# Optimization experiments

Hardware: AMD Instinct MI355X
Metric: run time of the kernel (lower is better)

## Reference

```python
import jax, jax.numpy as jnp
import numpy as np

D_MODEL = 256
N_LEVELS = 4
N_HEADS = 8
N_POINTS = 4
D_HEAD = D_MODEL // N_HEADS  # 32
BATCH = 8
SHAPES = np.array([[64, 64], [32, 32], [16, 16], [8, 8]], dtype=np.int32)
LEN_IN = int((SHAPES[:, 0] * SHAPES[:, 1]).sum())  # 5440
LEN_Q = LEN_IN
STARTS = np.concatenate([[0], np.cumsum(SHAPES[:, 0] * SHAPES[:, 1])[:-1]]).astype(np.int32)


def _offset_bias():
    # faithful _reset_parameters grid init for sampling_offsets bias
    thetas = np.arange(N_HEADS, dtype=np.float64) * (2.0 * np.pi / N_HEADS)
    grid = np.stack([np.cos(thetas), np.sin(thetas)], -1)
    grid = grid / np.abs(grid).max(-1, keepdims=True)
    grid = np.tile(grid[:, None, None, :], (1, N_LEVELS, N_POINTS, 1))
    grid = grid * (np.arange(N_POINTS) + 1)[None, None, :, None]
    return jnp.asarray(grid.reshape(-1), dtype=jnp.float32)


def setup_inputs() -> dict:
    key = jax.random.key(0)
    ks = jax.random.split(key, 8)
    s = 1.0 / np.sqrt(D_MODEL)
    return {
        "query": jax.random.normal(ks[0], (BATCH, LEN_Q, D_MODEL), jnp.float32),
        "reference_points": jax.random.uniform(ks[1], (BATCH, LEN_Q, N_LEVELS, 2), jnp.float32),
        "input_flatten": jax.random.normal(ks[2], (BATCH, LEN_IN, D_MODEL), jnp.float32),
        "input_spatial_shapes": jnp.asarray(SHAPES),
        "input_level_start_index": jnp.asarray(STARTS),
        "W_val": jax.random.normal(ks[3], (D_MODEL, D_MODEL), jnp.float32) * s,
        "b_val": jnp.zeros((D_MODEL,), jnp.float32),
        "W_off": jax.random.normal(ks[4], (D_MODEL, N_HEADS * N_LEVELS * N_POINTS * 2), jnp.float32) * 0.01,
        "b_off": _offset_bias(),
        "W_attn": jax.random.normal(ks[5], (D_MODEL, N_HEADS * N_LEVELS * N_POINTS), jnp.float32) * s,
        "b_attn": jnp.zeros((N_HEADS * N_LEVELS * N_POINTS,), jnp.float32),
        "W_out": jax.random.normal(ks[6], (D_MODEL, D_MODEL), jnp.float32) * s,
        "b_out": jnp.zeros((D_MODEL,), jnp.float32),
    }


def _ms_deform_attn_core(value, shapes_np, starts_np, sampling_locations, attention_weights):
    # value: (N, Lin, Hn, d); sampling_locations: (N, Lq, Hn, L, P, 2) in [0,1]
    # attention_weights: (N, Lq, Hn, L, P)
    n, lq = sampling_locations.shape[:2]
    value_t = jnp.transpose(value, (0, 2, 1, 3))  # (N, Hn, Lin, d)
    out = jnp.zeros((n, N_HEADS, lq, value.shape[-1]), value.dtype)
    for lvl in range(N_LEVELS):
        H, W = int(shapes_np[lvl, 0]), int(shapes_np[lvl, 1])
        st = int(starts_np[lvl])
        v = value_t[:, :, st:st + H * W]  # (N, Hn, H*W, d)
        loc = jnp.transpose(sampling_locations[:, :, :, lvl], (0, 2, 1, 3, 4))  # (N, Hn, Lq, P, 2)
        x = loc[..., 0] * W - 0.5
        y = loc[..., 1] * H - 0.5
        x0 = jnp.floor(x).astype(jnp.int32)
        y0 = jnp.floor(y).astype(jnp.int32)
        lx = x - x0
        ly = y - y0
        x1, y1 = x0 + 1, y0 + 1

        def gather(yc, xc):
            valid = (yc >= 0) & (yc < H) & (xc >= 0) & (xc < W)
            idx = jnp.clip(yc, 0, H - 1) * W + jnp.clip(xc, 0, W - 1)
            idx = idx.reshape(n, N_HEADS, -1)  # (N, Hn, Lq*P)
            g = jnp.take_along_axis(v, idx[..., None], axis=2)  # (N, Hn, Lq*P, d)
            return g * valid.reshape(n, N_HEADS, -1, 1)

        w00 = ((1 - lx) * (1 - ly)).reshape(n, N_HEADS, -1, 1)
        w01 = (lx * (1 - ly)).reshape(n, N_HEADS, -1, 1)
        w10 = ((1 - lx) * ly).reshape(n, N_HEADS, -1, 1)
        w11 = (lx * ly).reshape(n, N_HEADS, -1, 1)
        samp = (gather(y0, x0) * w00 + gather(y0, x1) * w01 +
                gather(y1, x0) * w10 + gather(y1, x1) * w11)
        samp = samp.reshape(n, N_HEADS, lq, N_POINTS, -1)
        aw = jnp.transpose(attention_weights[:, :, :, lvl], (0, 2, 1, 3))  # (N, Hn, Lq, P)
        out = out + (samp * aw[..., None]).sum(axis=3)
    return jnp.transpose(out, (0, 2, 1, 3)).reshape(n, lq, -1)


def reference(query, reference_points, input_flatten, input_spatial_shapes,
              input_level_start_index, W_val, b_val, W_off, b_off,
              W_attn, b_attn, W_out, b_out):
    shapes_np = np.asarray(input_spatial_shapes)
    starts_np = np.asarray(input_level_start_index)
    n, lq, _ = query.shape
    lin = input_flatten.shape[1]

    value = (input_flatten @ W_val + b_val).reshape(n, lin, N_HEADS, D_HEAD)
    off = (query @ W_off + b_off).reshape(n, lq, N_HEADS, N_LEVELS, N_POINTS, 2)
    attn = jax.nn.softmax((query @ W_attn + b_attn).reshape(n, lq, N_HEADS, N_LEVELS * N_POINTS), axis=-1)
    attn = attn.reshape(n, lq, N_HEADS, N_LEVELS, N_POINTS)

    # normalizer: (L, 2) as [W, H]
    normalizer = jnp.stack([input_spatial_shapes[:, 1], input_spatial_shapes[:, 0]], -1).astype(query.dtype)
    loc = reference_points[:, :, None, :, None, :] + off / normalizer[None, None, None, :, None, :]

    out = _ms_deform_attn_core(value, shapes_np, starts_np, loc, attn)
    return out @ W_out + b_out
```

## Files before the change

kernel.cpp:

```cpp
#include <hip/hip_runtime.h>

typedef unsigned short ushort;
typedef unsigned int uint;
typedef __bf16 bf16x8 __attribute__((ext_vector_type(8)));
typedef float floatx4 __attribute__((ext_vector_type(4)));
typedef float floatx2 __attribute__((ext_vector_type(2)));
typedef ushort ushort8 __attribute__((ext_vector_type(8)));
typedef uint uintx4 __attribute__((ext_vector_type(4)));

constexpr int LQ = 5440;
constexpr int ROWS = 43520;

__device__ __forceinline__ ushort f2b(float f) {
  union { float f; uint i; } v; v.f = f;
  uint r = v.i + 0x7FFFu + ((v.i >> 16) & 1u);
  return (ushort)(r >> 16);
}
__device__ __forceinline__ float blo(uint u) {
  union { uint i; float f; } v; v.i = u << 16; return v.f;
}
__device__ __forceinline__ float bhi(uint u) {
  union { uint i; float f; } v; v.i = u & 0xFFFF0000u; return v.f;
}

__global__ __launch_bounds__(256) void wcast_kernel(
    const float* __restrict__ Wv, const float* __restrict__ Wo,
    const float* __restrict__ Wa, const float* __restrict__ Wu,
    ushort* __restrict__ Wt) {
  int k = threadIdx.x;
  int n = blockIdx.x;
  int m = blockIdx.y;
  const float* src = (m == 0) ? Wv : (m == 1) ? Wo : (m == 2) ? Wa : Wu;
  int N = (m == 2) ? 128 : 256;
  if (n >= N) return;
  size_t off = (size_t)m * 65536 - ((m == 3) ? 32768 : 0);
  Wt[off + (size_t)n * 256 + k] = f2b(src[(size_t)k * N + n]);
}

template<bool F2B>
__device__ __forceinline__ void tile64_mainloop(
    const void* __restrict__ Av, const ushort* __restrict__ Bt,
    int row_base, int n0, ushort* At, ushort* Bs, floatx4 (&acc)[4][2]) {
  const int t = threadIdx.x;
  const int lane = t & 63, wv = t >> 6;
#pragma unroll
  for (int i = 0; i < 4; ++i)
#pragma unroll
    for (int j = 0; j < 2; ++j) acc[i][j] = floatx4{0.f, 0.f, 0.f, 0.f};

  for (int k0 = 0; k0 < 256; k0 += 32) {
    {
      int r = t >> 2, q = t & 3;
      int slot = ((r >> 4) * 64 + q * 16 + (r & 15)) * 8;
      if (F2B) {
        const float* ap = (const float*)Av + (size_t)(row_base + r) * 256 + k0 + q * 8;
        float4 a0 = *(const float4*)ap, a1 = *(const float4*)(ap + 4);
        ushort8 u;
        u[0] = f2b(a0.x); u[1] = f2b(a0.y); u[2] = f2b(a0.z); u[3] = f2b(a0.w);
        u[4] = f2b(a1.x); u[5] = f2b(a1.y); u[6] = f2b(a1.z); u[7] = f2b(a1.w);
        *(ushort8*)&At[slot] = u;
      } else {
        const ushort* ap = (const ushort*)Av + (size_t)(row_base + r) * 256 + k0 + q * 8;
        *(ushort8*)&At[slot] = *(const ushort8*)ap;
      }
    }
#pragma unroll
    for (int i = 0; i < 2; ++i) {
      int item = t + 256 * i;
      int nr = item >> 2, q = item & 3;
      int slot = ((nr >> 4) * 64 + q * 16 + (nr & 15)) * 8;
      *(ushort8*)&Bs[slot] = *(const ushort8*)(Bt + (size_t)(n0 + nr) * 256 + k0 + q * 8);
    }
    __syncthreads();
    bf16x8 af[4], bf[2];
#pragma unroll
    for (int ti = 0; ti < 4; ++ti)
      af[ti] = *(const bf16x8*)&At[(ti * 64 + lane) * 8];
#pragma unroll
    for (int tjj = 0; tjj < 2; ++tjj)
      bf[tjj] = *(const bf16x8*)&Bs[((2 * wv + tjj) * 64 + lane) * 8];
#pragma unroll
    for (int ti = 0; ti < 4; ++ti)
#pragma unroll
      for (int tjj = 0; tjj < 2; ++tjj)
        acc[ti][tjj] = __builtin_amdgcn_mfma_f32_16x16x32_bf16(af[ti], bf[tjj], acc[ti][tjj], 0, 0, 0);
    __syncthreads();
  }
}

__global__ __launch_bounds__(256) void gemm_val64(
    const float* __restrict__ X, const ushort* __restrict__ WtV,
    const float* __restrict__ bval, ushort* __restrict__ value16) {
  __shared__ ushort At[2048];
  __shared__ ushort Bs[4096];
  floatx4 acc[4][2];
  int row_base = blockIdx.x * 64, n0 = blockIdx.y * 128;
  tile64_mainloop<true>(X, WtV, row_base, n0, At, Bs, acc);
  const int t = threadIdx.x, lane = t & 63, wv = t >> 6;
  const int quad = lane >> 4, l15 = lane & 15;
#pragma unroll
  for (int tjj = 0; tjj < 2; ++tjj) {
    int gcol = n0 + (2 * wv + tjj) * 16 + l15;
    float b = bval[gcol];
#pragma unroll
    for (int ti = 0; ti < 4; ++ti)
#pragma unroll
      for (int reg = 0; reg < 4; ++reg) {
        int grow = row_base + ti * 16 + quad * 4 + reg;
        value16[(size_t)grow * 256 + gcol] = f2b(acc[ti][tjj][reg] + b);
      }
  }
}

__global__ __launch_bounds__(256) void gemm_oa_kernel(
    const float* __restrict__ Q, const ushort* __restrict__ WtOA,
    const float* __restrict__ boff, const float* __restrict__ battn,
    const float* __restrict__ refp, uint4* __restrict__ tblq) {
  __shared__ ushort At[2048];
  __shared__ ushort Bs[3072];
  const int t = threadIdx.x;
  const int lane = t & 63, wv = t >> 6;
  const int quad = lane >> 4, l15 = lane & 15;
  const int bx = blockIdx.x;
  const int row_base = (bx % 680) * 64;
  const int hp = bx / 680;
  floatx4 accO[4], accA[2];
#pragma unroll
  for (int p = 0; p < 4; ++p) accO[p] = floatx4{0.f, 0.f, 0.f, 0.f};
#pragma unroll
  for (int q = 0; q < 2; ++q) accA[q] = floatx4{0.f, 0.f, 0.f, 0.f};

  for (int k0 = 0; k0 < 256; k0 += 32) {
    {
      int r = t >> 2, q = t & 3;
      const float* ap = Q + (size_t)(row_base + r) * 256 + k0 + q * 8;
      float4 a0 = *(const float4*)ap, a1 = *(const float4*)(ap + 4);
      ushort8 u;
      u[0] = f2b(a0.x); u[1] = f2b(a0.y); u[2] = f2b(a0.z); u[3] = f2b(a0.w);
      u[4] = f2b(a1.x); u[5] = f2b(a1.y); u[6] = f2b(a1.z); u[7] = f2b(a1.w);
      *(ushort8*)&At[((r >> 4) * 64 + q * 16 + (r & 15)) * 8] = u;
    }
#pragma unroll
    for (int i = 0; i < 2; ++i) {
      int item = t + 256 * i;
      if (item < 384) {
        int nrl = item >> 2, q = item & 3;
        int grow_ = (nrl < 64) ? (hp * 64 + nrl) : (256 + hp * 32 + (nrl - 64));
        *(ushort8*)&Bs[((nrl >> 4) * 64 + q * 16 + (nrl & 15)) * 8] =
            *(const ushort8*)(WtOA + (size_t)grow_ * 256 + k0 + q * 8);
      }
    }
    __syncthreads();
    bf16x8 af = *(const bf16x8*)&At[(wv * 64 + lane) * 8];
#pragma unroll
    for (int p = 0; p < 4; ++p) {
      bf16x8 bf = *(const bf16x8*)&Bs[(p * 64 + lane) * 8];
      accO[p] = __builtin_amdgcn_mfma_f32_16x16x32_bf16(af, bf, accO[p], 0, 0, 0);
    }
#pragma unroll
    for (int q = 0; q < 2; ++q) {
      bf16x8 bf = *(const bf16x8*)&Bs[((4 + q) * 64 + lane) * 8];
      accA[q] = __builtin_amdgcn_mfma_f32_16x16x32_bf16(af, bf, accA[q], 0, 0, 0);
    }
    __syncthreads();
  }

  const int lp = l15, l = lp >> 2;
  const int wd = 64 >> l;
  const int st = (l == 0) ? 0 : (l == 1) ? 4096 : (l == 2) ? 5120 : 5376;
  const float lw = (float)wd;
  const int src = (quad << 4) | (2 * (lp & 7));
  float boO[4], boA[2];
#pragma unroll
  for (int p = 0; p < 4; ++p) boO[p] = boff[(4 * hp + p) * 16 + l15];
#pragma unroll
  for (int q = 0; q < 2; ++q) boA[q] = battn[(2 * hp + q) * 16 + l15];

#pragma unroll
  for (int reg = 0; reg < 4; ++reg) {
    int grow = row_base + wv * 16 + quad * 4 + reg;
    float rx = refp[(size_t)grow * 8 + l * 2];
    float ry = refp[(size_t)grow * 8 + l * 2 + 1];
#pragma unroll
    for (int hh = 0; hh < 2; ++hh) {
      int h = 2 * hp + hh;
      float xa = accA[hh][reg] + boA[hh];
      float m = xa;
      m = fmaxf(m, __shfl_xor(m, 1, 64));
      m = fmaxf(m, __shfl_xor(m, 2, 64));
      m = fmaxf(m, __shfl_xor(m, 4, 64));
      m = fmaxf(m, __shfl_xor(m, 8, 64));
      float e = __expf(xa - m);
      float ssum = e;
      ssum += __shfl_xor(ssum, 1, 64);
      ssum += __shfl_xor(ssum, 2, 64);
      ssum += __shfl_xor(ssum, 4, 64);
      ssum += __shfl_xor(ssum, 8, 64);
      float aw = e / ssum;
      float v0 = accO[2 * hh][reg] + boO[2 * hh];
      float v1 = accO[2 * hh + 1][reg] + boO[2 * hh + 1];
      float x_lo = __shfl(v0, src, 64),     x_hi = __shfl(v1, src, 64);
      float y_lo = __shfl(v0, src | 1, 64), y_hi = __shfl(v1, src | 1, 64);
      float xo = (lp < 8) ? x_lo : x_hi;
      float yo = (lp < 8) ? y_lo : y_hi;
      float X = rx * lw + xo - 0.5f;
      float Y = ry * lw + yo - 0.5f;
      float fx = floorf(X), fy = floorf(Y);
      float lx = X - fx, ly = Y - fy;
      int x0 = (int)fx, y0 = (int)fy, x1 = x0 + 1, y1 = y0 + 1;
      int cx0 = min(max(x0, 0), wd - 1), cx1 = min(max(x1, 0), wd - 1);
      int cy0 = min(max(y0, 0), wd - 1), cy1 = min(max(y1, 0), wd - 1);
      float vx0 = (x0 >= 0 && x0 < wd) ? 1.f : 0.f;
      float vx1 = (x1 >= 0 && x1 < wd) ? 1.f : 0.f;
      float vy0 = (y0 >= 0 && y0 < wd) ? 1.f : 0.f;
      float vy1 = (y1 >= 0 && y1 < wd) ? 1.f : 0.f;
      float g00 = (1.f - lx) * (1.f - ly) * vx0 * vy0 * aw;
      float g01 = lx * (1.f - ly) * vx1 * vy0 * aw;
      float g10 = (1.f - lx) * ly * vx0 * vy1 * aw;
      float g11 = lx * ly * vx1 * vy1 * aw;
      uint i00 = st + cy0 * wd + cx0, i01 = st + cy0 * wd + cx1;
      uint i10 = st + cy1 * wd + cx0, i11 = st + cy1 * wd + cx1;
      uint4 ov;
      ov.x = i00 | (i01 << 16);
      ov.y = i10 | (i11 << 16);
      ov.z = (uint)f2b(g00) | ((uint)f2b(g01) << 16);
      ov.w = (uint)f2b(g10) | ((uint)f2b(g11) << 16);
      tblq[((size_t)grow * 8 + h) * 16 + lp] = ov;
    }
  }
}

__device__ __forceinline__ void accum4p(uint wz, uint ww, const uint2* __restrict__ vv,
                                        floatx2& x01, floatx2& x23) {
  const float ws[4] = {blo(wz), bhi(wz), blo(ww), bhi(ww)};
#pragma unroll
  for (int j = 0; j < 4; ++j) {
    floatx2 wj = {ws[j], ws[j]};
    floatx2 p = {blo(vv[j].x), bhi(vv[j].x)};
    floatx2 q = {blo(vv[j].y), bhi(vv[j].y)};
    x01 = __builtin_elementwise_fma(wj, p, x01);
    x23 = __builtin_elementwise_fma(wj, q, x23);
  }
}

__device__ __forceinline__ void consume_pair(
    const uintx4& S0, const uintx4& S1, const uintx4& S2, const uintx4& S3,
    const uint2* __restrict__ V, int brow0, int h, int s, int g,
    uint* __restrict__ coreo32) {
  floatx2 a01 = {0.f, 0.f}, a23 = {0.f, 0.f};
  floatx2 c01 = {0.f, 0.f}, c23 = {0.f, 0.f};
  accum4p(S0[2], S0[3], V + 0,  a01, a23);
  accum4p(S1[2], S1[3], V + 4,  a01, a23);
  accum4p(S2[2], S2[3], V + 8,  c01, c23);
  accum4p(S3[2], S3[3], V + 12, c01, c23);
#pragma unroll
  for (int m = 8; m <= 32; m <<= 1) {
    a01.x += __shfl_xor(a01.x, m, 64);
    a01.y += __shfl_xor(a01.y, m, 64);
    a23.x += __shfl_xor(a23.x, m, 64);
    a23.y += __shfl_xor(a23.y, m, 64);
    c01.x += __shfl_xor(c01.x, m, 64);
    c01.y += __shfl_xor(c01.y, m, 64);
    c23.x += __shfl_xor(c23.x, m, 64);
    c23.y += __shfl_xor(c23.y, m, 64);
  }
  if (s == 0) {
    uint2 o0, o1;
    o0.x = (uint)f2b(a01.x) | ((uint)f2b(a01.y) << 16);
    o0.y = (uint)f2b(a23.x) | ((uint)f2b(a23.y) << 16);
    o1.x = (uint)f2b(c01.x) | ((uint)f2b(c01.y) << 16);
    o1.y = (uint)f2b(c23.x) | ((uint)f2b(c23.y) << 16);
    *(uint2*)(coreo32 + (size_t)brow0 * 128 + h * 16 + g * 2) = o0;
    *(uint2*)(coreo32 + (size_t)(brow0 + 1) * 128 + h * 16 + g * 2) = o1;
  }
}

__global__ __launch_bounds__(512) void core_kernel(
    const ushort* __restrict__ value16, const uint4* __restrict__ tblq,
    uint* __restrict__ coreo32) {
  const int bx = blockIdx.x;
  const int b = bx & 7;
  const int tile = bx >> 3;
  const int t = threadIdx.x;
  const int h = t >> 6, lane = t & 63;
  const int s = lane >> 3, g = lane & 7;
  const uint g8 = (uint)(g << 3);
  const char* vbh = (const char*)value16 + (size_t)b * (LQ * 512) + (h << 6);
  const uintx4* tb = (const uintx4*)tblq;
  const int row0 = b * LQ + tile * 4;
  const size_t sb = ((size_t)row0 * 8 + h) * 16 + s;

  uintx4 A0 = __builtin_nontemporal_load(tb + sb);
  uintx4 A1 = __builtin_nontemporal_load(tb + sb + 8);
  uintx4 A2 = __builtin_nontemporal_load(tb + sb + 128);
  uintx4 A3 = __builtin_nontemporal_load(tb + sb + 136);
  uintx4 B0 = __builtin_nontemporal_load(tb + sb + 256);
  uintx4 B1 = __builtin_nontemporal_load(tb + sb + 264);
  uintx4 B2 = __builtin_nontemporal_load(tb + sb + 384);
  uintx4 B3 = __builtin_nontemporal_load(tb + sb + 392);

  uint2 VA[16], VB[16];
#define GL(d, idx16) d = *(const uint2*)(vbh + (((uint)(idx16) << 9) + g8))
  GL(VA[0],  (A0[0] & 0xFFFFu)); GL(VA[1],  (A0[0] >> 16));
  GL(VA[2],  (A0[1] & 0xFFFFu)); GL(VA[3],  (A0[1] >> 16));
  GL(VA[4],  (A1[0] & 0xFFFFu)); GL(VA[5],  (A1[0] >> 16));
  GL(VA[6],  (A1[1] & 0xFFFFu)); GL(VA[7],  (A1[1] >> 16));
  GL(VA[8],  (A2[0] & 0xFFFFu)); GL(VA[9],  (A2[0] >> 16));
  GL(VA[10], (A2[1] & 0xFFFFu)); GL(VA[11], (A2[1] >> 16));
  GL(VA[12], (A3[0] & 0xFFFFu)); GL(VA[13], (A3[0] >> 16));
  GL(VA[14], (A3[1] & 0xFFFFu)); GL(VA[15], (A3[1] >> 16));
  GL(VB[0],  (B0[0] & 0xFFFFu)); GL(VB[1],  (B0[0] >> 16));
  GL(VB[2],  (B0[1] & 0xFFFFu)); GL(VB[3],  (B0[1] >> 16));
  GL(VB[4],  (B1[0] & 0xFFFFu)); GL(VB[5],  (B1[0] >> 16));
  GL(VB[6],  (B1[1] & 0xFFFFu)); GL(VB[7],  (B1[1] >> 16));
  GL(VB[8],  (B2[0] & 0xFFFFu)); GL(VB[9],  (B2[0] >> 16));
  GL(VB[10], (B2[1] & 0xFFFFu)); GL(VB[11], (B2[1] >> 16));
  GL(VB[12], (B3[0] & 0xFFFFu)); GL(VB[13], (B3[0] >> 16));
  GL(VB[14], (B3[1] & 0xFFFFu)); GL(VB[15], (B3[1] >> 16));
#undef GL

  consume_pair(A0, A1, A2, A3, VA, row0,     h, s, g, coreo32);
  consume_pair(B0, B1, B2, B3, VB, row0 + 2, h, s, g, coreo32);
}

__global__ __launch_bounds__(256) void gemm_out64(
    const ushort* __restrict__ C, const ushort* __restrict__ WtU,
    const float* __restrict__ bout, float* __restrict__ out) {
  __shared__ ushort At[2048];
  __shared__ ushort Bs[4096];
  floatx4 acc[4][2];
  int row_base = blockIdx.x * 64, n0 = blockIdx.y * 128;
  tile64_mainloop<false>(C, WtU, row_base, n0, At, Bs, acc);
  const int t = threadIdx.x, lane = t & 63, wv = t >> 6;
  const int quad = lane >> 4, l15 = lane & 15;
#pragma unroll
  for (int tjj = 0; tjj < 2; ++tjj) {
    int gcol = n0 + (2 * wv + tjj) * 16 + l15;
    float b = bout[gcol];
#pragma unroll
    for (int ti = 0; ti < 4; ++ti)
#pragma unroll
      for (int reg = 0; reg < 4; ++reg) {
        int grow = row_base + ti * 16 + quad * 4 + reg;
        out[(size_t)grow * 256 + gcol] = acc[ti][tjj][reg] + b;
      }
  }
}

extern "C" void kernel_launch(void* const* d_in, const int* in_sizes, int n_in,
                              void* d_out, int out_size, void* d_ws, size_t ws_size,
                              hipStream_t stream) {
  const float* query  = (const float*)d_in[0];
  const float* refp   = (const float*)d_in[1];
  const float* inpf   = (const float*)d_in[2];
  const float* W_val  = (const float*)d_in[5];
  const float* b_val  = (const float*)d_in[6];
  const float* W_off  = (const float*)d_in[7];
  const float* b_off  = (const float*)d_in[8];
  const float* W_attn = (const float*)d_in[9];
  const float* b_attn = (const float*)d_in[10];
  const float* W_out  = (const float*)d_in[11];
  const float* b_out  = (const float*)d_in[12];

  char* ws = (char*)d_ws;
  ushort* Wt    = (ushort*)ws;
  ushort* value = (ushort*)(ws + 1048576);
  uint4*  tbl   = (uint4*)(ws + 23330816);
  ushort* coreo = (ushort*)(ws + 112459776);

  dim3 blk(256);
  wcast_kernel<<<dim3(256, 4), blk, 0, stream>>>(W_val, W_off, W_attn, W_out, Wt);
  gemm_val64  <<<dim3(680, 2), blk, 0, stream>>>(inpf, Wt, b_val, value);
  gemm_oa_kernel<<<dim3(2720), blk, 0, stream>>>(query, Wt + 65536, b_off, b_attn, refp, tbl);
  core_kernel <<<dim3(10880), dim3(512), 0, stream>>>(value, tbl, (uint*)coreo);
  gemm_out64  <<<dim3(680, 2), blk, 0, stream>>>(coreo, Wt + 163840, b_out, (float*)d_out);
}
```

Baseline: 329.4 us.

## Widen GEMM tiles to full N and use direct global-to-LDS loads

The value and output projection GEMMs now compute all 256 output columns per block instead of splitting N across two blocks. The fp32 input is therefore read and converted to bf16 once rather than twice. Weight tiles (and the bf16 A tile in the output GEMM) are now loaded with global_load_lds straight into shared memory in the MFMA layout, bypassing registers. In exchange, accumulator registers double, the grid halves to 680 blocks, and LDS use grows, which may reduce occupancy.

Measured after the change: 334.4 us. No clear change (+1.5%).

```diff
diff --git a/kernel.cpp b/kernel.cpp
--- a/kernel.cpp
+++ b/kernel.cpp
@@ -21,6 +21,11 @@
 }
 __device__ __forceinline__ float bhi(uint u) {
   union { uint i; float f; } v; v.i = u & 0xFFFF0000u; return v.f;
+}
+__device__ __forceinline__ void glds16(const ushort* g, ushort* l) {
+  __builtin_amdgcn_global_load_lds(
+      (const __attribute__((address_space(1))) void*)g,
+      (__attribute__((address_space(3))) void*)l, 16, 0, 0);
 }
 
 __global__ __launch_bounds__(256) void wcast_kernel(
@@ -37,77 +42,66 @@
   Wt[off + (size_t)n * 256 + k] = f2b(src[(size_t)k * N + n]);
 }
 
-template<bool F2B>
-__device__ __forceinline__ void tile64_mainloop(
-    const void* __restrict__ Av, const ushort* __restrict__ Bt,
-    int row_base, int n0, ushort* At, ushort* Bs, floatx4 (&acc)[4][2]) {
-  const int t = threadIdx.x;
-  const int lane = t & 63, wv = t >> 6;
-#pragma unroll
-  for (int i = 0; i < 4; ++i)
-#pragma unroll
-    for (int j = 0; j < 2; ++j) acc[i][j] = floatx4{0.f, 0.f, 0.f, 0.f};
-
-  for (int k0 = 0; k0 < 256; k0 += 32) {
-    {
-      int r = t >> 2, q = t & 3;
-      int slot = ((r >> 4) * 64 + q * 16 + (r & 15)) * 8;
-      if (F2B) {
-        const float* ap = (const float*)Av + (size_t)(row_base + r) * 256 + k0 + q * 8;
-        float4 a0 = *(const float4*)ap, a1 = *(const float4*)(ap + 4);
-        ushort8 u;
-        u[0] = f2b(a0.x); u[1] = f2b(a0.y); u[2] = f2b(a0.z); u[3] = f2b(a0.w);
-        u[4] = f2b(a1.x); u[5] = f2b(a1.y); u[6] = f2b(a1.z); u[7] = f2b(a1.w);
-        *(ushort8*)&At[slot] = u;
-      } else {
-        const ushort* ap = (const ushort*)Av + (size_t)(row_base + r) * 256 + k0 + q * 8;
-        *(ushort8*)&At[slot] = *(const ushort8*)ap;
-      }
-    }
-#pragma unroll
-    for (int i = 0; i < 2; ++i) {
-      int item = t + 256 * i;
-      int nr = item >> 2, q = item & 3;
-      int slot = ((nr >> 4) * 64 + q * 16 + (nr & 15)) * 8;
-      *(ushort8*)&Bs[slot] = *(const ushort8*)(Bt + (size_t)(n0 + nr) * 256 + k0 + q * 8);
-    }
-    __syncthreads();
-    bf16x8 af[4], bf[2];
-#pragma unroll
-    for (int ti = 0; ti < 4; ++ti)
-      af[ti] = *(const bf16x8*)&At[(ti * 64 + lane) * 8];
-#pragma unroll
-    for (int tjj = 0; tjj < 2; ++tjj)
-      bf[tjj] = *(const bf16x8*)&Bs[((2 * wv + tjj) * 64 + lane) * 8];
-#pragma unroll
-    for (int ti = 0; ti < 4; ++ti)
-#pragma unroll
-      for (int tjj = 0; tjj < 2; ++tjj)
-        acc[ti][tjj] = __builtin_amdgcn_mfma_f32_16x16x32_bf16(af[ti], bf[tjj], acc[ti][tjj], 0, 0, 0);
-    __syncthreads();
-  }
-}
-
 __global__ __launch_bounds__(256) void gemm_val64(
     const float* __restrict__ X, const ushort* __restrict__ WtV,
     const float* __restrict__ bval, ushort* __restrict__ value16) {
   __shared__ ushort At[2048];
-  __shared__ ushort Bs[4096];
-  floatx4 acc[4][2];
-  int row_base = blockIdx.x * 64, n0 = blockIdx.y * 128;
-  tile64_mainloop<true>(X, WtV, row_base, n0, At, Bs, acc);
+  __shared__ ushort Bs[8192];
   const int t = threadIdx.x, lane = t & 63, wv = t >> 6;
+  const int row_base = blockIdx.x * 64;
+  floatx4 acc[4][4];
+#pragma unroll
+  for (int i = 0; i < 4; ++i)
+#pragma unroll
+    for (int j = 0; j < 4; ++j) acc[i][j] = floatx4{0.f, 0.f, 0.f, 0.f};
+
+  const int r = t >> 2, q = t & 3;
+  const float* ap = X + (size_t)(row_base + r) * 256 + q * 8;
+  ushort* aslot = &At[((r >> 4) * 64 + q * 16 + (r & 15)) * 8];
+  const ushort* bsrc[4];
+#pragma unroll
+  for (int i = 0; i < 4; ++i) {
+    int l = t + 256 * i;
+    int nt = l >> 6, qq = (l >> 4) & 3, n15 = l & 15;
+    bsrc[i] = WtV + (size_t)(nt * 16 + n15) * 256 + qq * 8;
+  }
+
+  for (int k0 = 0; k0 < 256; k0 += 32) {
+#pragma unroll
+    for (int i = 0; i < 4; ++i) glds16(bsrc[i] + k0, &Bs[(t + 256 * i) * 8]);
+    {
+      float4 a0 = *(const float4*)(ap + k0), a1 = *(const float4*)(ap + k0 + 4);
+      ushort8 u;
+      u[0] = f2b(a0.x); u[1] = f2b(a0.y); u[2] = f2b(a0.z); u[3] = f2b(a0.w);
+      u[4] = f2b(a1.x); u[5] = f2b(a1.y); u[6] = f2b(a1.z); u[7] = f2b(a1.w);
+      *(ushort8*)aslot = u;
+    }
+    __syncthreads();
+    bf16x8 af[4], bf[4];
+#pragma unroll
+    for (int ti = 0; ti < 4; ++ti)
+      af[ti] = *(const bf16x8*)&At[(ti * 64 + lane) * 8];
+#pragma unroll
+    for (int tj = 0; tj < 4; ++tj)
+      bf[tj] = *(const bf16x8*)&Bs[((4 * wv + tj) * 64 + lane) * 8];
+#pragma unroll
+    for (int ti = 0; ti < 4; ++ti)
+#pragma unroll
+      for (int tj = 0; tj < 4; ++tj)
+        acc[ti][tj] = __builtin_amdgcn_mfma_f32_16x16x32_bf16(af[ti], bf[tj], acc[ti][tj], 0, 0, 0);
+    __syncthreads();
+  }
   const int quad = lane >> 4, l15 = lane & 15;
 #pragma unroll
-  for (int tjj = 0; tjj < 2; ++tjj) {
-    int gcol = n0 + (2 * wv + tjj) * 16 + l15;
+  for (int tj = 0; tj < 4; ++tj) {
+    int gcol = (4 * wv + tj) * 16 + l15;
     float b = bval[gcol];
 #pragma unroll
     for (int ti = 0; ti < 4; ++ti)
 #pragma unroll
       for (int reg = 0; reg < 4; ++reg) {
         int grow = row_base + ti * 16 + quad * 4 + reg;
-        value16[(size_t)grow * 256 + gcol] = f2b(acc[ti][tjj][reg] + b);
+        value16[(size_t)grow * 256 + gcol] = f2b(acc[ti][tj][reg] + b);
       }
   }
 }
@@ -130,25 +124,34 @@
 #pragma unroll
   for (int q = 0; q < 2; ++q) accA[q] = floatx4{0.f, 0.f, 0.f, 0.f};
 
+  const int r = t >> 2, q = t & 3;
+  const float* ap = Q + (size_t)(row_base + r) * 256 + q * 8;
+  ushort* aslot = &At[((r >> 4) * 64 + q * 16 + (r & 15)) * 8];
+  const ushort* osrc0;
+  const ushort* osrc1 = nullptr;
+  {
+    int nt = t >> 6, qq = (t >> 4) & 3, n15 = t & 15;
+    int nr = nt * 16 + n15;
+    int grow_ = (nr < 64) ? (hp * 64 + nr) : (256 + hp * 32 + (nr - 64));
+    osrc0 = WtOA + (size_t)grow_ * 256 + qq * 8;
+  }
+  if (t < 128) {
+    int l = t + 256;
+    int nt = l >> 6, qq = (l >> 4) & 3, n15 = l & 15;
+    int nr = nt * 16 + n15;
+    int grow_ = 256 + hp * 32 + (nr - 64);
+    osrc1 = WtOA + (size_t)grow_ * 256 + qq * 8;
+  }
+
   for (int k0 = 0; k0 < 256; k0 += 32) {
+    glds16(osrc0 + k0, &Bs[t * 8]);
+    if (t < 128) glds16(osrc1 + k0, &Bs[(t + 256) * 8]);
     {
-      int r = t >> 2, q = t & 3;
-      const float* ap = Q + (size_t)(row_base + r) * 256 + k0 + q * 8;
-      float4 a0 = *(const float4*)ap, a1 = *(const float4*)(ap + 4);
+      float4 a0 = *(const float4*)(ap + k0), a1 = *(const float4*)(ap + k0 + 4);
       ushort8 u;
       u[0] = f2b(a0.x); u[1] = f2b(a0.y); u[2] = f2b(a0.z); u[3] = f2b(a0.w);
       u[4] = f2b(a1.x); u[5] = f2b(a1.y); u[6] = f2b(a1.z); u[7] = f2b(a1.w);
-      *(ushort8*)&At[((r >> 4) * 64 + q * 16 + (r & 15)) * 8] = u;
-    }
-#pragma unroll
-    for (int i = 0; i < 2; ++i) {
-      int item = t + 256 * i;
-      if (item < 384) {
-        int nrl = item >> 2, q = item & 3;
-        int grow_ = (nrl < 64) ? (hp * 64 + nrl) : (256 + hp * 32 + (nrl - 64));
-        *(ushort8*)&Bs[((nrl >> 4) * 64 + q * 16 + (nrl & 15)) * 8] =
-            *(const ushort8*)(WtOA + (size_t)grow_ * 256 + k0 + q * 8);
-      }
+      *(ushort8*)aslot = u;
     }
     __syncthreads();
     bf16x8 af = *(const bf16x8*)&At[(wv * 64 + lane) * 8];
@@ -158,9 +161,9 @@
       accO[p] = __builtin_amdgcn_mfma_f32_16x16x32_bf16(af, bf, accO[p], 0, 0, 0);
     }
 #pragma unroll
-    for (int q = 0; q < 2; ++q) {
-      bf16x8 bf = *(const bf16x8*)&Bs[((4 + q) * 64 + lane) * 8];
-      accA[q] = __builtin_amdgcn_mfma_f32_16x16x32_bf16(af, bf, accA[q], 0, 0, 0);
+    for (int qk = 0; qk < 2; ++qk) {
+      bf16x8 bf = *(const bf16x8*)&Bs[((4 + qk) * 64 + lane) * 8];
+      accA[qk] = __builtin_amdgcn_mfma_f32_16x16x32_bf16(af, bf, accA[qk], 0, 0, 0);
     }
     __syncthreads();
   }
@@ -174,7 +177,7 @@
 #pragma unroll
   for (int p = 0; p < 4; ++p) boO[p] = boff[(4 * hp + p) * 16 + l15];
 #pragma unroll
-  for (int q = 0; q < 2; ++q) boA[q] = battn[(2 * hp + q) * 16 + l15];
+  for (int qk = 0; qk < 2; ++qk) boA[qk] = battn[(2 * hp + qk) * 16 + l15];
 
 #pragma unroll
   for (int reg = 0; reg < 4; ++reg) {
@@ -327,22 +330,58 @@
     const ushort* __restrict__ C, const ushort* __restrict__ WtU,
     const float* __restrict__ bout, float* __restrict__ out) {
   __shared__ ushort At[2048];
-  __shared__ ushort Bs[4096];
-  floatx4 acc[4][2];
-  int row_base = blockIdx.x * 64, n0 = blockIdx.y * 128;
-  tile64_mainloop<false>(C, WtU, row_base, n0, At, Bs, acc);
+  __shared__ ushort Bs[8192];
   const int t = threadIdx.x, lane = t & 63, wv = t >> 6;
+  const int row_base = blockIdx.x * 64;
+  floatx4 acc[4][4];
+#pragma unroll
+  for (int i = 0; i < 4; ++i)
+#pragma unroll
+    for (int j = 0; j < 4; ++j) acc[i][j] = floatx4{0.f, 0.f, 0.f, 0.f};
+
+  const ushort* asrc;
+  {
+    int mt = t >> 6, qq = (t >> 4) & 3, r15 = t & 15;
+    asrc = C + (size_t)(row_base + mt * 16 + r15) * 256 + qq * 8;
+  }
+  const ushort* bsrc[4];
+#pragma unroll
+  for (int i = 0; i < 4; ++i) {
+    int l = t + 256 * i;
+    int nt = l >> 6, qq = (l >> 4) & 3, n15 = l & 15;
+    bsrc[i] = WtU + (size_t)(nt * 16 + n15) * 256 + qq * 8;
+  }
+
+  for (int k0 = 0; k0 < 256; k0 += 32) {
+    glds16(asrc + k0, &At[t * 8]);
+#pragma unroll
+    for (int i = 0; i < 4; ++i) glds16(bsrc[i] + k0, &Bs[(t + 256 * i) * 8]);
+    __syncthreads();
+    bf16x8 af[4], bf[4];
+#pragma unroll
+    for (int ti = 0; ti < 4; ++ti)
+      af[ti] = *(const bf16x8*)&At[(ti * 64 + lane) * 8];
+#pragma unroll
+    for (int tj = 0; tj < 4; ++tj)
+      bf[tj] = *(const bf16x8*)&Bs[((4 * wv + tj) * 64 + lane) * 8];
+#pragma unroll
+    for (int ti = 0; ti < 4; ++ti)
+#pragma unroll
+      for (int tj = 0; tj < 4; ++tj)
+        acc[ti][tj] = __builtin_amdgcn_mfma_f32_16x16x32_bf16(af[ti], bf[tj], acc[ti][tj], 0, 0, 0);
+    __syncthreads();
+  }
   const int quad = lane >> 4, l15 = lane & 15;
 #pragma unroll
-  for (int tjj = 0; tjj < 2; ++tjj) {
-    int gcol = n0 + (2 * wv + tjj) * 16 + l15;
+  for (int tj = 0; tj < 4; ++tj) {
+    int gcol = (4 * wv + tj) * 16 + l15;
     float b = bout[gcol];
 #pragma unroll
     for (int ti = 0; ti < 4; ++ti)
 #pragma unroll
       for (int reg = 0; reg < 4; ++reg) {
         int grow = row_base + ti * 16 + quad * 4 + reg;
-        out[(size_t)grow * 256 + gcol] = acc[ti][tjj][reg] + b;
+        out[(size_t)grow * 256 + gcol] = acc[ti][tj][reg] + b;
       }
   }
 }
@@ -370,8 +409,8 @@
 
   dim3 blk(256);
   wcast_kernel<<<dim3(256, 4), blk, 0, stream>>>(W_val, W_off, W_attn, W_out, Wt);
-  gemm_val64  <<<dim3(680, 2), blk, 0, stream>>>(inpf, Wt, b_val, value);
+  gemm_val64  <<<dim3(680), blk, 0, stream>>>(inpf, Wt, b_val, value);
   gemm_oa_kernel<<<dim3(2720), blk, 0, stream>>>(query, Wt + 65536, b_off, b_attn, refp, tbl);
   core_kernel <<<dim3(10880), dim3(512), 0, stream>>>(value, tbl, (uint*)coreo);
-  gemm_out64  <<<dim3(680, 2), blk, 0, stream>>>(coreo, Wt + 163840, b_out, (float*)d_out);
-}
+  gemm_out64  <<<dim3(680), blk, 0, stream>>>(coreo, Wt + 163840, b_out, (float*)d_out);
+}
```
